# Performance work log

Measured on AMD Instinct MI355X. Metric: run time of the kernel, lower is better.

The kernel has to match this reference:

```python
import jax, jax.numpy as jnp
import numpy as np

B, OBS, NH, LAT = 8192, 256, 2048, 128

def setup_inputs() -> dict:
    key = jax.random.key(0)
    k1, k2, k3, k4, k5, k6 = jax.random.split(key, 6)
    s1 = 1.0 / np.sqrt(OBS + NH)
    s2 = 1.0 / np.sqrt(NH)
    return {
        "x": jax.random.normal(k1, (B, OBS), dtype=jnp.float32),
        "h": jax.random.normal(k2, (B, NH), dtype=jnp.float32),
        "W_i2h": jax.random.normal(k3, (NH, OBS + NH), dtype=jnp.float32) * s1,
        "b_i2h": jax.random.normal(k4, (NH,), dtype=jnp.float32) * s1,
        "W_h2o": jax.random.normal(k5, (2 * LAT, NH), dtype=jnp.float32) * s2,
        "b_h2o": jax.random.normal(k6, (2 * LAT,), dtype=jnp.float32) * s2,
    }

def reference(x, h, W_i2h, b_i2h, W_h2o, b_h2o):
    # combined = cat((x, h), dim=1)  -> [B, OBS+NH]
    combined = jnp.concatenate([x, h], axis=1)
    # h_new = tanh(i2h(combined));  Linear is y = x @ W.T + b
    h_new = jnp.tanh(combined @ W_i2h.T + b_i2h)
    out = h_new @ W_h2o.T + b_h2o  # [B, 2*LAT]
    return (out, h_new)
```

## Files before the change

### kernel.cpp

```cpp
#include <hip/hip_runtime.h>
#include <hip/hip_bf16.h>
#include <cstdint>

using bf16 = __hip_bfloat16;
typedef __attribute__((ext_vector_type(8))) short short8;
typedef __attribute__((ext_vector_type(4))) float floatx4;
typedef __attribute__((ext_vector_type(16))) float floatx16;

static constexpr int BATCH = 8192;
static constexpr int K1    = 2304;
static constexpr int N1    = 2048;
static constexpr int K2    = 2048;
static constexpr int N2    = 256;

__device__ __forceinline__ void gload_lds16(const void* g, void* l) {
  __builtin_amdgcn_global_load_lds(
      (const __attribute__((address_space(1))) void*)g,
      (__attribute__((address_space(3))) void*)l, 16, 0, 0);
}

__device__ __forceinline__ float fast_tanh(float x) {
  float e = __builtin_amdgcn_exp2f(x * 2.8853900817779268f);
  return 1.0f - 2.0f * __builtin_amdgcn_rcpf(e + 1.0f);
}

__device__ __forceinline__ short8 cvt8(const float* src) {
  float4 a = ((const float4*)src)[0];
  float4 b = ((const float4*)src)[1];
  union { short8 v; bf16 e[8]; } u;
  u.e[0] = __float2bfloat16(a.x); u.e[1] = __float2bfloat16(a.y);
  u.e[2] = __float2bfloat16(a.z); u.e[3] = __float2bfloat16(a.w);
  u.e[4] = __float2bfloat16(b.x); u.e[5] = __float2bfloat16(b.y);
  u.e[6] = __float2bfloat16(b.z); u.e[7] = __float2bfloat16(b.w);
  return u.v;
}

static constexpr int SEG0 = BATCH * (K1 / 8);
static constexpr int SEG1 = N1 * K1 / 8;
static constexpr int SEG2 = N2 * K2 / 8;
static constexpr int SEG3 = BATCH * N2 / 4;
__global__ __launch_bounds__(256) void prep(
    const float* __restrict__ x, const float* __restrict__ h,
    const float* __restrict__ W1, const float* __restrict__ W2,
    const float* __restrict__ b2,
    bf16* __restrict__ comb, bf16* __restrict__ W1b, bf16* __restrict__ W2b,
    float* __restrict__ out) {
  int i = blockIdx.x * 256 + threadIdx.x;
  if (i < SEG0) {
    int row  = i / 288;
    int slot = i - row * 288;
    const float* src = (slot < 32) ? (x + (size_t)row * 256 + slot * 8)
                                   : (h + (size_t)row * 2048 + (slot - 32) * 8);
    *(short8*)(comb + (size_t)row * 2304 + slot * 8) = cvt8(src);
  } else if (i < SEG0 + SEG1) {
    int j = i - SEG0;
    *(short8*)(W1b + (size_t)j * 8) = cvt8(W1 + (size_t)j * 8);
  } else if (i < SEG0 + SEG1 + SEG2) {
    int j = i - (SEG0 + SEG1);
    *(short8*)(W2b + (size_t)j * 8) = cvt8(W2 + (size_t)j * 8);
  } else {
    int j = i - (SEG0 + SEG1 + SEG2);
    ((float4*)out)[j] = ((const float4*)b2)[j & 63];
  }
}

__global__ __launch_bounds__(256) void gemm1_tanh(
    const bf16* __restrict__ A, const bf16* __restrict__ W,
    const float* __restrict__ bias,
    float* __restrict__ hf32, bf16* __restrict__ hb16) {
  __shared__ bf16 As[128 * 64];
  __shared__ bf16 Bs[128 * 64];
  const int t    = threadIdx.x;
  const int lane = t & 63;
  const int wave = t >> 6;
  const int wm   = (wave & 1) * 64;
  const int wn   = (wave >> 1) * 64;
  const int r31  = lane & 31;
  const int half = lane >> 5;
  const int srow = t >> 3;
  const int sc   = t & 7;

  const size_t Abase = (size_t)blockIdx.x * 128 * K1;
  const size_t Bbase = (size_t)blockIdx.y * 128 * K1;

  floatx16 acc[2][2];
#pragma unroll
  for (int i = 0; i < 2; i++)
#pragma unroll
    for (int j = 0; j < 2; j++)
#pragma unroll
      for (int r = 0; r < 16; r++) acc[i][j][r] = 0.f;

  for (int kt = 0; kt < K1 / 64; ++kt) {
    const int k0 = kt * 64;
    __syncthreads();
#pragma unroll
    for (int it = 0; it < 4; ++it) {
      int row = it * 32 + srow;
      int gc  = k0 + ((sc ^ (row & 7)) << 3);
      gload_lds16(A + Abase + (size_t)row * K1 + gc,
                  (char*)As + it * 4096 + t * 16);
    }
#pragma unroll
    for (int it = 0; it < 4; ++it) {
      int row = it * 32 + srow;
      int gc  = k0 + ((sc ^ (row & 7)) << 3);
      gload_lds16(W + Bbase + (size_t)row * K1 + gc,
                  (char*)Bs + it * 4096 + t * 16);
    }
    __syncthreads();
#pragma unroll
    for (int ks = 0; ks < 4; ++ks) {
      short8 af[2], bfr[2];
      const int kq = ks * 2 + half;
#pragma unroll
      for (int mt = 0; mt < 2; ++mt) {
        int row = wm + mt * 32 + r31;
        af[mt] = *(const short8*)((const char*)As + row * 128 +
                                  ((kq ^ (row & 7)) << 4));
      }
#pragma unroll
      for (int nt = 0; nt < 2; ++nt) {
        int row = wn + nt * 32 + r31;
        bfr[nt] = *(const short8*)((const char*)Bs + row * 128 +
                                   ((kq ^ (row & 7)) << 4));
      }
#pragma unroll
      for (int mt = 0; mt < 2; ++mt)
#pragma unroll
        for (int nt = 0; nt < 2; ++nt)
          acc[mt][nt] = __builtin_amdgcn_mfma_f32_32x32x16_bf16(
              af[mt], bfr[nt], acc[mt][nt], 0, 0, 0);
    }
  }

  const int gcol0 = blockIdx.y * 128 + wn;
  float bv[2];
#pragma unroll
  for (int nt = 0; nt < 2; ++nt) bv[nt] = bias[gcol0 + nt * 32 + r31];
  const size_t grow0 = (size_t)blockIdx.x * 128 + wm;
#pragma unroll
  for (int mt = 0; mt < 2; ++mt) {
#pragma unroll
    for (int r = 0; r < 16; ++r) {
      size_t gr = grow0 + mt * 32 + (r & 3) + 8 * (r >> 2) + 4 * half;
      size_t rb = gr * (size_t)N1;
#pragma unroll
      for (int nt = 0; nt < 2; ++nt) {
        int gc = gcol0 + nt * 32 + r31;
        float v = fast_tanh(acc[mt][nt][r] + bv[nt]);
        hf32[rb + gc] = v;
        hb16[rb + gc] = __float2bfloat16(v);
      }
    }
  }
}

__global__ __launch_bounds__(256) void gemm2_out(
    const bf16* __restrict__ A, const bf16* __restrict__ W,
    float* __restrict__ out) {
  __shared__ bf16 As[32 * 64];
  __shared__ bf16 Bs[256 * 64];
  const int t    = threadIdx.x;
  const int lane = t & 63;
  const int wave = t >> 6;
  const int quad = lane >> 4;
  const int r15  = lane & 15;
  const int srow = t >> 3;
  const int sc   = t & 7;

  const int mrow0 = blockIdx.x * 32;
  const int kbase = blockIdx.y * (K2 / 4);

  floatx4 acc[2][4];
  const floatx4 z = {0.f, 0.f, 0.f, 0.f};
#pragma unroll
  for (int i = 0; i < 2; i++)
#pragma unroll
    for (int j = 0; j < 4; j++) acc[i][j] = z;

  for (int kt = 0; kt < 8; ++kt) {
    const int k0 = kbase + kt * 64;
    __syncthreads();
    {
      int row = srow;
      int gc  = k0 + ((sc ^ (row & 7)) << 3);
      gload_lds16(A + (size_t)(mrow0 + row) * K2 + gc, (char*)As + t * 16);
    }
#pragma unroll
    for (int it = 0; it < 8; ++it) {
      int row = it * 32 + srow;
      int gc  = k0 + ((sc ^ (row & 7)) << 3);
      gload_lds16(W + (size_t)row * K2 + gc,
                  (char*)Bs + it * 4096 + t * 16);
    }
    __syncthreads();
#pragma unroll
    for (int ks = 0; ks < 2; ++ks) {
      short8 af[2], bfr[4];
      const int kq = ks * 4 + quad;
#pragma unroll
      for (int mt = 0; mt < 2; ++mt) {
        int row = mt * 16 + r15;
        af[mt] = *(const short8*)((const char*)As + row * 128 +
                                  ((kq ^ (row & 7)) << 4));
      }
#pragma unroll
      for (int nt = 0; nt < 4; ++nt) {
        int row = wave * 64 + nt * 16 + r15;
        bfr[nt] = *(const short8*)((const char*)Bs + row * 128 +
                                   ((kq ^ (row & 7)) << 4));
      }
#pragma unroll
      for (int mt = 0; mt < 2; ++mt)
#pragma unroll
        for (int nt = 0; nt < 4; ++nt)
          acc[mt][nt] = __builtin_amdgcn_mfma_f32_16x16x32_bf16(
              af[mt], bfr[nt], acc[mt][nt], 0, 0, 0);
    }
  }

  const int gcol0 = wave * 64;
#pragma unroll
  for (int mt = 0; mt < 2; ++mt) {
#pragma unroll
    for (int i = 0; i < 4; ++i) {
      size_t gr = (size_t)mrow0 + mt * 16 + quad * 4 + i;
      size_t rb = gr * (size_t)N2;
#pragma unroll
      for (int nt = 0; nt < 4; ++nt) {
        int gc = gcol0 + nt * 16 + r15;
        unsafeAtomicAdd(&out[rb + gc], acc[mt][nt][i]);
      }
    }
  }
}

extern "C" void kernel_launch(void* const* d_in, const int* in_sizes, int n_in,
                              void* d_out, int out_size, void* d_ws,
                              size_t ws_size, hipStream_t stream) {
  const float* x     = (const float*)d_in[0];
  const float* h     = (const float*)d_in[1];
  const float* W_i2h = (const float*)d_in[2];
  const float* b_i2h = (const float*)d_in[3];
  const float* W_h2o = (const float*)d_in[4];
  const float* b_h2o = (const float*)d_in[5];

  float* out       = (float*)d_out;
  float* hnew_f32  = out + (size_t)BATCH * N2;

  bf16* comb   = (bf16*)d_ws;
  bf16* Wi2h_b = comb + (size_t)BATCH * K1;
  bf16* Wh2o_b = Wi2h_b + (size_t)N1 * K1;
  bf16* hnew_b = Wh2o_b + (size_t)N2 * K2;

  prep<<<(SEG0 + SEG1 + SEG2 + SEG3) / 256, 256, 0, stream>>>(
      x, h, W_i2h, W_h2o, b_h2o, comb, Wi2h_b, Wh2o_b, out);

  gemm1_tanh<<<dim3(BATCH / 128, N1 / 128), 256, 0, stream>>>(
      comb, Wi2h_b, b_i2h, hnew_f32, hnew_b);

  gemm2_out<<<dim3(BATCH / 32, 4), 256, 0, stream>>>(hnew_b, Wh2o_b, out);
}
```

Before: 283.1 us.

## Fuse activation fp32-to-bf16 conversion into GEMM1 A-tile loading

Removes the prep-kernel pass that concatenated x and h and converted them to a bf16 workspace. GEMM1 now reads the fp32 x/h rows directly, converts them to bf16 in registers and stores them to swizzled LDS. This saves a full write and re-read of the 8192x2304 bf16 combined matrix. In exchange, each of the 16 column blocks re-reads the A tiles in fp32, doubling A-load bytes per block, and the loads go through registers instead of the direct global-to-LDS path.

```diff
diff --git a/kernel.cpp b/kernel.cpp
--- a/kernel.cpp
+++ b/kernel.cpp
@@ -35,38 +35,29 @@
   return u.v;
 }
 
-static constexpr int SEG0 = BATCH * (K1 / 8);
 static constexpr int SEG1 = N1 * K1 / 8;
 static constexpr int SEG2 = N2 * K2 / 8;
 static constexpr int SEG3 = BATCH * N2 / 4;
 __global__ __launch_bounds__(256) void prep(
-    const float* __restrict__ x, const float* __restrict__ h,
     const float* __restrict__ W1, const float* __restrict__ W2,
     const float* __restrict__ b2,
-    bf16* __restrict__ comb, bf16* __restrict__ W1b, bf16* __restrict__ W2b,
+    bf16* __restrict__ W1b, bf16* __restrict__ W2b,
     float* __restrict__ out) {
   int i = blockIdx.x * 256 + threadIdx.x;
-  if (i < SEG0) {
-    int row  = i / 288;
-    int slot = i - row * 288;
-    const float* src = (slot < 32) ? (x + (size_t)row * 256 + slot * 8)
-                                   : (h + (size_t)row * 2048 + (slot - 32) * 8);
-    *(short8*)(comb + (size_t)row * 2304 + slot * 8) = cvt8(src);
-  } else if (i < SEG0 + SEG1) {
-    int j = i - SEG0;
-    *(short8*)(W1b + (size_t)j * 8) = cvt8(W1 + (size_t)j * 8);
-  } else if (i < SEG0 + SEG1 + SEG2) {
-    int j = i - (SEG0 + SEG1);
+  if (i < SEG1) {
+    *(short8*)(W1b + (size_t)i * 8) = cvt8(W1 + (size_t)i * 8);
+  } else if (i < SEG1 + SEG2) {
+    int j = i - SEG1;
     *(short8*)(W2b + (size_t)j * 8) = cvt8(W2 + (size_t)j * 8);
   } else {
-    int j = i - (SEG0 + SEG1 + SEG2);
+    int j = i - (SEG1 + SEG2);
     ((float4*)out)[j] = ((const float4*)b2)[j & 63];
   }
 }
 
 __global__ __launch_bounds__(256) void gemm1_tanh(
-    const bf16* __restrict__ A, const bf16* __restrict__ W,
-    const float* __restrict__ bias,
+    const float* __restrict__ x, const float* __restrict__ h,
+    const bf16* __restrict__ W, const float* __restrict__ bias,
     float* __restrict__ hf32, bf16* __restrict__ hb16) {
   __shared__ bf16 As[128 * 64];
   __shared__ bf16 Bs[128 * 64];
@@ -79,8 +70,9 @@
   const int half = lane >> 5;
   const int srow = t >> 3;
   const int sc   = t & 7;
-
-  const size_t Abase = (size_t)blockIdx.x * 128 * K1;
+  const int cchunk = sc ^ (srow & 7);
+
+  const int    mrow0 = blockIdx.x * 128;
   const size_t Bbase = (size_t)blockIdx.y * 128 * K1;
 
   floatx16 acc[2][2];
@@ -93,18 +85,21 @@
 
   for (int kt = 0; kt < K1 / 64; ++kt) {
     const int k0 = kt * 64;
-    __syncthreads();
+    const float* srcb;
+    size_t stride;
+    if (kt < 4) { srcb = x + kt * 64;         stride = 256;  }
+    else        { srcb = h + (kt - 4) * 64;   stride = 2048; }
+    __syncthreads();
+#pragma unroll
+    for (int it = 0; it < 4; ++it) {
+      int row_g = mrow0 + it * 32 + srow;
+      short8 v = cvt8(srcb + (size_t)row_g * stride + cchunk * 8);
+      *(short8*)((char*)As + it * 4096 + t * 16) = v;
+    }
 #pragma unroll
     for (int it = 0; it < 4; ++it) {
       int row = it * 32 + srow;
-      int gc  = k0 + ((sc ^ (row & 7)) << 3);
-      gload_lds16(A + Abase + (size_t)row * K1 + gc,
-                  (char*)As + it * 4096 + t * 16);
-    }
-#pragma unroll
-    for (int it = 0; it < 4; ++it) {
-      int row = it * 32 + srow;
-      int gc  = k0 + ((sc ^ (row & 7)) << 3);
+      int gc  = k0 + (cchunk << 3);
       gload_lds16(W + Bbase + (size_t)row * K1 + gc,
                   (char*)Bs + it * 4096 + t * 16);
     }
@@ -138,7 +133,7 @@
   float bv[2];
 #pragma unroll
   for (int nt = 0; nt < 2; ++nt) bv[nt] = bias[gcol0 + nt * 32 + r31];
-  const size_t grow0 = (size_t)blockIdx.x * 128 + wm;
+  const size_t grow0 = (size_t)mrow0 + wm;
 #pragma unroll
   for (int mt = 0; mt < 2; ++mt) {
 #pragma unroll
@@ -249,16 +244,15 @@
   float* out       = (float*)d_out;
   float* hnew_f32  = out + (size_t)BATCH * N2;
 
-  bf16* comb   = (bf16*)d_ws;
-  bf16* Wi2h_b = comb + (size_t)BATCH * K1;
+  bf16* Wi2h_b = (bf16*)d_ws;
   bf16* Wh2o_b = Wi2h_b + (size_t)N1 * K1;
   bf16* hnew_b = Wh2o_b + (size_t)N2 * K2;
 
-  prep<<<(SEG0 + SEG1 + SEG2 + SEG3) / 256, 256, 0, stream>>>(
-      x, h, W_i2h, W_h2o, b_h2o, comb, Wi2h_b, Wh2o_b, out);
+  prep<<<(SEG1 + SEG2 + SEG3) / 256, 256, 0, stream>>>(
+      W_i2h, W_h2o, b_h2o, Wi2h_b, Wh2o_b, out);
 
   gemm1_tanh<<<dim3(BATCH / 128, N1 / 128), 256, 0, stream>>>(
-      comb, Wi2h_b, b_i2h, hnew_f32, hnew_b);
+      x, h, Wi2h_b, b_i2h, hnew_f32, hnew_b);
 
   gemm2_out<<<dim3(BATCH / 32, 4), 256, 0, stream>>>(hnew_b, Wh2o_b, out);
 }
```

Measured after the change: 302.5 us. 6.9% more time.
